# Performance work log

Measured on AMD Instinct MI355X. Metric: run time of the kernel, lower is better.

Reference implementation:

```python
import jax, jax.numpy as jnp
import numpy as np

EPS = 1e-5
B, C_IN, T_IN = 512, 12, 5000
NF, HID, LAT = 32, 64, 32


def setup_inputs() -> dict:
    key = jax.random.key(0)
    ks = jax.random.split(key, 12)
    inp = {
        "x": jax.random.normal(ks[0], (B, C_IN, T_IN), dtype=jnp.float32),
        # conv stack
        "conv1_w": jax.random.normal(ks[1], (32, C_IN, 50), dtype=jnp.float32) * 0.05,
        "conv1_b": jnp.zeros((32,), dtype=jnp.float32),
        "bn1_g": jnp.ones((32,), dtype=jnp.float32),
        "bn1_b": jnp.zeros((32,), dtype=jnp.float32),
        "conv2_w": jax.random.normal(ks[2], (NF, 32, 25), dtype=jnp.float32) * 0.05,
        "conv2_b": jnp.zeros((NF,), dtype=jnp.float32),
        "bn2_g": jnp.ones((NF,), dtype=jnp.float32),
        "bn2_b": jnp.zeros((NF,), dtype=jnp.float32),
        # input projection + layernorm
        "proj_w": jax.random.normal(ks[3], (LAT, NF), dtype=jnp.float32) * 0.1,
        "proj_b": jnp.zeros((LAT,), dtype=jnp.float32),
        "ln_g": jnp.ones((LAT,), dtype=jnp.float32),
        "ln_b": jnp.zeros((LAT,), dtype=jnp.float32),
        # PLRNN recurrence params
        "A": jnp.eye(LAT, dtype=jnp.float32) * 0.9,
        "W": jax.random.normal(ks[4], (LAT, HID), dtype=jnp.float32) * 0.1,
        "h_bias": jnp.zeros((HID,), dtype=jnp.float32),
        # output projection
        "out_w": jax.random.normal(ks[5], (LAT, LAT), dtype=jnp.float32) * 0.1,
        "out_b": jnp.zeros((LAT,), dtype=jnp.float32),
    }
    return inp


def _conv1d(x, w, b, stride):
    # x: [B, C, T], w: [O, I, K]
    y = jax.lax.conv_general_dilated(
        x, w, window_strides=(stride,), padding="VALID",
        dimension_numbers=("NCH", "OIH", "NCH"))
    return y + b[None, :, None]


def _batchnorm_train(x, g, b):
    # training-mode BN over (batch, time) per channel; x: [B, C, T]
    mean = jnp.mean(x, axis=(0, 2), keepdims=True)
    var = jnp.mean((x - mean) ** 2, axis=(0, 2), keepdims=True)
    return (x - mean) * jax.lax.rsqrt(var + EPS) * g[None, :, None] + b[None, :, None]


def _layernorm(x, g, b):
    mean = jnp.mean(x, axis=-1, keepdims=True)
    var = jnp.mean((x - mean) ** 2, axis=-1, keepdims=True)
    return (x - mean) * jax.lax.rsqrt(var + EPS) * g + b


def reference(x, conv1_w, conv1_b, bn1_g, bn1_b, conv2_w, conv2_b, bn2_g, bn2_b,
              proj_w, proj_b, ln_g, ln_b, A, W, h_bias, out_w, out_b):
    # conv front-end
    y = jax.nn.relu(_batchnorm_train(_conv1d(x, conv1_w, conv1_b, 10), bn1_g, bn1_b))
    y = jax.nn.relu(_batchnorm_train(_conv1d(y, conv2_w, conv2_b, 5), bn2_g, bn2_b))
    y = jnp.transpose(y, (0, 2, 1))  # [B, T, NF], T = 95

    # input projection + LN, vectorized over all timesteps
    xt = _layernorm(jnp.einsum("btf,lf->btl", y, proj_w) + proj_b, ln_g, ln_b)  # [B, T, L]
    xs = jnp.transpose(xt, (1, 0, 2))  # [T, B, L] for scan

    def step(h, x_t):
        # h: [B, L]
        linear = h @ A.T
        nonlinear = jax.nn.relu(h @ W + h_bias) @ W.T
        h_new = linear + nonlinear + x_t
        return h_new, h_new

    h0 = jnp.zeros((x.shape[0], A.shape[0]), dtype=x.dtype)
    _, outputs = jax.lax.scan(step, h0, xs)  # [T, B, L]

    pooled = jnp.mean(outputs, axis=0)  # [B, L]
    return pooled @ out_w.T + out_b
```

## Files before the change

### kernel.cpp

```cpp
#include <hip/hip_runtime.h>

#define NB    512
#define CIN   12
#define TIN   5000
#define C1    32
#define T1    496
#define T2    95
#define LATD  32
#define HIDD  64

#define OFS_STATS 0
#define OFS_W1P   256
#define OFS_W2P   19456
#define OFS_Y1    45056
#define OFS_Y2    8171520
#define OFS_XS    OFS_Y1

__global__ void prep_kernel(const float* __restrict__ w1, const float* __restrict__ w2,
                            float* __restrict__ ws) {
    int idx = blockIdx.x * 256 + threadIdx.x;
    if (idx < 256) ws[idx] = 0.f;
    int j = idx - 256;
    if (j >= 0 && j < 19200) {
        int ic = j / 1600, r = j % 1600, k = r / 32, oc = r % 32;
        ws[OFS_W1P + j] = w1[oc * 600 + ic * 50 + k];
    }
    int j2 = idx - 19456;
    if (j2 >= 0 && j2 < 25600) {
        int ic = j2 / 800, r = j2 % 800, k = r / 32, oc = r % 32;
        ws[OFS_W2P + j2] = w2[oc * 800 + ic * 25 + k];
    }
}

__global__ __launch_bounds__(128, 2) void conv1_kernel(const float* __restrict__ x,
                                                       const float* __restrict__ b1,
                                                       float* __restrict__ ws) {
    const float* w1p = ws + OFS_W1P;
    float* y1 = ws + OFS_Y1;
    float* stats = ws + OFS_STATS;
    int b  = blockIdx.x >> 1;
    int t0 = (blockIdx.x & 1) * 256;
    int tid = threadIdx.x;
    int ocg = tid & 3, tg = tid >> 2;
    int oc0 = ocg * 8, lt0 = tg * 8;
    int xbase = 82 * tg;

    __shared__ __align__(16) float xs_s[2][2664];
    __shared__ __align__(16) float ws_s[2][1600];
    __shared__ float sred[128];

    float acc[8][8];
#pragma unroll
    for (int a = 0; a < 8; ++a)
#pragma unroll
        for (int c = 0; c < 8; ++c) acc[a][c] = 0.f;

    const float* xb = x + (size_t)b * (CIN * TIN) + t0 * 10;
    int nvalid = TIN - t0 * 10;

    float4 px[6];
    float4 pw[4];

    auto fetch = [&](int ic) {
#pragma unroll
        for (int j = 0; j < 6; ++j) {
            int i = tid + j * 128;
            if (i < 650) {
                int src = 4 * i;
                const float* gp = xb + ic * TIN + src;
                float4 v;
                if (src + 4 <= nvalid) {
                    v = *(const float4*)gp;
                } else {
                    v.x = (src + 0 < nvalid) ? gp[0] : 0.f;
                    v.y = (src + 1 < nvalid) ? gp[1] : 0.f;
                    v.z = (src + 2 < nvalid) ? gp[2] : 0.f;
                    v.w = (src + 3 < nvalid) ? gp[3] : 0.f;
                }
                px[j] = v;
            }
        }
#pragma unroll
        for (int j = 0; j < 4; ++j) {
            int i = tid + j * 128;
            if (i < 400) pw[j] = *(const float4*)(w1p + ic * 1600 + 4 * i);
        }
    };

    fetch(0);
    for (int ic = 0; ic < CIN; ++ic) {
        int cur = ic & 1;
        __syncthreads();
#pragma unroll
        for (int j = 0; j < 6; ++j) {
            int i = tid + j * 128;
            if (i < 650) {
                int src = 4 * i;
                int dst = src + (i / 20) * 2;
                float2 lo; lo.x = px[j].x; lo.y = px[j].y;
                float2 hi; hi.x = px[j].z; hi.y = px[j].w;
                *(float2*)&xs_s[cur][dst]     = lo;
                *(float2*)&xs_s[cur][dst + 2] = hi;
            }
        }
#pragma unroll
        for (int j = 0; j < 4; ++j) {
            int i = tid + j * 128;
            if (i < 400) *(float4*)&ws_s[cur][4 * i] = pw[j];
        }
        if (ic + 1 < CIN) fetch(ic + 1);
        __syncthreads();

#pragma unroll 1
        for (int kp = 0; kp < 25; ++kp) {
            const int k = kp * 2;
            const float* wr = &ws_s[cur][k * 32 + oc0];
            float4 w00 = *(const float4*)wr;
            float4 w01 = *(const float4*)(wr + 4);
            float4 w10 = *(const float4*)(wr + 32);
            float4 w11 = *(const float4*)(wr + 36);
            float2 xv[8];
#pragma unroll
            for (int jt = 0; jt < 8; ++jt) {
                int r = jt * 10 + k;
                int ad = xbase + r + ((r >= 80) ? 2 : 0);
                xv[jt] = *(const float2*)&xs_s[cur][ad];
            }
            float wk[8]  = {w00.x, w00.y, w00.z, w00.w, w01.x, w01.y, w01.z, w01.w};
            float wk1[8] = {w10.x, w10.y, w10.z, w10.w, w11.x, w11.y, w11.z, w11.w};
#pragma unroll
            for (int jo = 0; jo < 8; ++jo)
#pragma unroll
                for (int jt = 0; jt < 8; ++jt)
                    acc[jo][jt] = fmaf(wk1[jo], xv[jt].y, fmaf(wk[jo], xv[jt].x, acc[jo][jt]));
        }
    }

    float bias[8];
#pragma unroll
    for (int jo = 0; jo < 8; ++jo) bias[jo] = b1[oc0 + jo];

    bool tvalid = (t0 + lt0) <= (T1 - 8);
    float psum[8], psq[8];
#pragma unroll
    for (int jo = 0; jo < 8; ++jo) {
        float s = 0.f, q = 0.f;
        if (tvalid) {
            float tmp[8];
#pragma unroll
            for (int jt = 0; jt < 8; ++jt) {
                float v = acc[jo][jt] + bias[jo];
                tmp[jt] = v; s += v; q = fmaf(v, v, q);
            }
            float* yrow = y1 + (size_t)(b * 32 + oc0 + jo) * T1 + t0 + lt0;
            float4 o0; o0.x = tmp[0]; o0.y = tmp[1]; o0.z = tmp[2]; o0.w = tmp[3];
            float4 o1; o1.x = tmp[4]; o1.y = tmp[5]; o1.z = tmp[6]; o1.w = tmp[7];
            *(float4*)yrow       = o0;
            *(float4*)(yrow + 4) = o1;
        }
        psum[jo] = s; psq[jo] = q;
    }
#pragma unroll
    for (int off = 32; off >= 4; off >>= 1) {
#pragma unroll
        for (int jo = 0; jo < 8; ++jo) {
            psum[jo] += __shfl_down(psum[jo], off, 64);
            psq[jo]  += __shfl_down(psq[jo],  off, 64);
        }
    }
    int lane = tid & 63, wvi = tid >> 6;
    if (lane < 4) {
#pragma unroll
        for (int jo = 0; jo < 8; ++jo) {
            sred[((wvi * 4 + lane) * 8 + jo) * 2 + 0] = psum[jo];
            sred[((wvi * 4 + lane) * 8 + jo) * 2 + 1] = psq[jo];
        }
    }
    __syncthreads();
    if (tid < 64) {
        int oc = tid >> 1, which = tid & 1;
        int og = oc >> 3, jo = oc & 7;
        float v = sred[((0 * 4 + og) * 8 + jo) * 2 + which] +
                  sred[((1 * 4 + og) * 8 + jo) * 2 + which];
        atomicAdd(&stats[which * 32 + oc], v);
    }
}

__global__ void bnstats_kernel(const float* __restrict__ g, const float* __restrict__ bparm,
                               float* __restrict__ ws, int base_in, int base_out, float invN) {
    int oc = threadIdx.x;
    if (oc < 32) {
        float* stats = ws + OFS_STATS;
        float mean = stats[base_in + oc] * invN;
        float var  = stats[base_in + 32 + oc] * invN - mean * mean;
        float s = g[oc] * rsqrtf(var + 1e-5f);
        stats[base_out + oc]      = s;
        stats[base_out + 32 + oc] = bparm[oc] - mean * s;
    }
}

__global__ __launch_bounds__(192, 2) void conv2_kernel(const float* __restrict__ b2,
                                                       float* __restrict__ ws) {
    const float* w2p = ws + OFS_W2P;
    const float* y1 = ws + OFS_Y1;
    float* y2 = ws + OFS_Y2;
    float* stats = ws + OFS_STATS;
    int b = blockIdx.x;
    int tid = threadIdx.x;
    int ocg = tid & 7, tg = tid >> 3;
    int oc0 = ocg * 4, lt0 = tg * 4;

    __shared__ __align__(16) float a1s[500];
    __shared__ __align__(16) float w2s[800];
    __shared__ float sred[192];

    float acc[4][4];
#pragma unroll
    for (int a = 0; a < 4; ++a)
#pragma unroll
        for (int c = 0; c < 4; ++c) acc[a][c] = 0.f;

    for (int ic = 0; ic < 32; ++ic) {
        __syncthreads();
        float s1  = stats[128 + ic];
        float sh1 = stats[160 + ic];
        const float* yrow = y1 + (size_t)(b * 32 + ic) * T1;
        for (int i = tid; i < 124; i += 192) {
            float4 v = *(const float4*)(yrow + 4 * i);
            v.x = fmaxf(fmaf(v.x, s1, sh1), 0.f);
            v.y = fmaxf(fmaf(v.y, s1, sh1), 0.f);
            v.z = fmaxf(fmaf(v.z, s1, sh1), 0.f);
            v.w = fmaxf(fmaf(v.w, s1, sh1), 0.f);
            *(float4*)&a1s[4 * i] = v;
        }
        for (int i = tid; i < 200; i += 192)
            *(float4*)&w2s[4 * i] = *(const float4*)(w2p + ic * 800 + 4 * i);
        __syncthreads();

#pragma unroll 1
        for (int kp = 0; kp < 12; ++kp) {
            const int k = kp * 2;
            float4 wA = *(const float4*)&w2s[k * 32 + oc0];
            float4 wB = *(const float4*)&w2s[(k + 1) * 32 + oc0];
            float x0[4], x1[4];
#pragma unroll
            for (int jt = 0; jt < 4; ++jt) {
                int a = 20 * tg + 5 * jt + k;
                x0[jt] = a1s[a]; x1[jt] = a1s[a + 1];
            }
            float wk[4]  = {wA.x, wA.y, wA.z, wA.w};
            float wk1[4] = {wB.x, wB.y, wB.z, wB.w};
#pragma unroll
            for (int jo = 0; jo < 4; ++jo)
#pragma unroll
                for (int jt = 0; jt < 4; ++jt)
                    acc[jo][jt] = fmaf(wk1[jo], x1[jt], fmaf(wk[jo], x0[jt], acc[jo][jt]));
        }
        float4 wT = *(const float4*)&w2s[24 * 32 + oc0];
        float wt[4] = {wT.x, wT.y, wT.z, wT.w};
#pragma unroll
        for (int jt = 0; jt < 4; ++jt) {
            float xt_ = a1s[20 * tg + 5 * jt + 24];
#pragma unroll
            for (int jo = 0; jo < 4; ++jo) acc[jo][jt] = fmaf(wt[jo], xt_, acc[jo][jt]);
        }
    }

    float bias[4];
#pragma unroll
    for (int jo = 0; jo < 4; ++jo) bias[jo] = b2[oc0 + jo];

    float psum[4], psq[4];
#pragma unroll
    for (int jo = 0; jo < 4; ++jo) {
        float s = 0.f, q = 0.f;
#pragma unroll
        for (int jt = 0; jt < 4; ++jt) {
            int t2 = lt0 + jt;
            if (t2 < T2) {
                float v = acc[jo][jt] + bias[jo];
                y2[(size_t)(b * 32 + oc0 + jo) * T2 + t2] = v;
                s += v; q = fmaf(v, v, q);
            }
        }
        psum[jo] = s; psq[jo] = q;
    }
#pragma unroll
    for (int off = 32; off >= 8; off >>= 1) {
#pragma unroll
        for (int jo = 0; jo < 4; ++jo) {
            psum[jo] += __shfl_down(psum[jo], off, 64);
            psq[jo]  += __shfl_down(psq[jo],  off, 64);
        }
    }
    int lane = tid & 63, wvi = tid >> 6;
    if (lane < 8) {
#pragma unroll
        for (int jo = 0; jo < 4; ++jo) {
            sred[((wvi * 8 + lane) * 4 + jo) * 2 + 0] = psum[jo];
            sred[((wvi * 8 + lane) * 4 + jo) * 2 + 1] = psq[jo];
        }
    }
    __syncthreads();
    if (tid < 64) {
        int oc = tid >> 1, which = tid & 1;
        int og = oc >> 2, jo = oc & 3;
        float v = 0.f;
#pragma unroll
        for (int w = 0; w < 3; ++w)
            v += sred[((w * 8 + og) * 4 + jo) * 2 + which];
        atomicAdd(&stats[64 + which * 32 + oc], v);
    }
}

__global__ __launch_bounds__(256, 2) void proj_kernel(const float* __restrict__ pw,
                                                      const float* __restrict__ pb,
                                                      const float* __restrict__ lng,
                                                      const float* __restrict__ lnb,
                                                      float* __restrict__ ws) {
    int b = blockIdx.x;
    int tid = threadIdx.x;
    __shared__ float a2s[3040];
    __shared__ float pws[1056];
    const float* stats = ws + OFS_STATS;
    const float* y2 = ws + OFS_Y2 + (size_t)b * (32 * T2);
    float* xsg = ws + OFS_XS;

    for (int f = 0; f < 32; ++f) {
        float s2  = stats[192 + f];
        float sh2 = stats[224 + f];
        if (tid < T2)
            a2s[f * T2 + tid] = fmaxf(fmaf(y2[f * T2 + tid], s2, sh2), 0.f);
    }
    for (int i = tid; i < 1024; i += 256)
        pws[(i >> 5) * 33 + (i & 31)] = pw[i];

    int l = tid & 31, ts = tid >> 5;
    float pbv = pb[l], lg = lng[l], lb = lnb[l];
    __syncthreads();

    for (int it = 0; it < 12; ++it) {
        int t = ts + 8 * it;
        if (t < T2) {
            float v = pbv;
#pragma unroll
            for (int f = 0; f < 32; ++f)
                v = fmaf(a2s[f * T2 + t], pws[l * 33 + f], v);
            float sum = v;
#pragma unroll
            for (int off = 16; off >= 1; off >>= 1) sum += __shfl_xor(sum, off, 64);
            float mean = sum * (1.f / 32.f);
            float d = v - mean;
            float q = d * d;
#pragma unroll
            for (int off = 16; off >= 1; off >>= 1) q += __shfl_xor(q, off, 64);
            float o = d * rsqrtf(q * (1.f / 32.f) + 1e-5f) * lg + lb;
            xsg[(size_t)t * (NB * 32) + b * 32 + l] = o;
        }
    }
}

__global__ __launch_bounds__(64)
__attribute__((amdgpu_waves_per_eu(1, 1)))
void scan_kernel(const float* __restrict__ Am,
                 const float* __restrict__ Wm,
                 const float* __restrict__ hbp,
                 const float* __restrict__ ow,
                 const float* __restrict__ ob,
                 const float* __restrict__ ws,
                 float* __restrict__ out) {
    int b = blockIdx.x;
    int lane = threadIdx.x;
    int l = lane & 31, half = lane >> 5;
    __shared__ __align__(16) float hs[32];
    __shared__ __align__(16) float hds[64];
    __shared__ float ows[1056];

    float Wc[32], WT[32], Ah[16];
#pragma unroll
    for (int j = 0; j < 32; ++j) Wc[j] = Wm[j * HIDD + lane];
#pragma unroll
    for (int m = 0; m < 32; ++m) WT[m] = Wm[l * HIDD + half * 32 + m];
#pragma unroll
    for (int j = 0; j < 16; ++j) Ah[j] = Am[l * 32 + half * 16 + j];
    float hbv = hbp[lane];
    for (int i = lane; i < 1024; i += 64)
        ows[(i >> 5) * 33 + (i & 31)] = ow[i];

    const float* xsg = ws + OFS_XS + b * 32;
    if (lane < 32) hs[l] = 0.f;
    float xv = xsg[l];
    float pool = 0.f;
    __syncthreads();

    for (int t = 0; t < T2; ++t) {
        __syncthreads();
        float4 hv[8];
#pragma unroll
        for (int q = 0; q < 8; ++q) hv[q] = *(const float4*)&hs[4 * q];
        float a0 = hbv, a1 = 0.f, a2 = 0.f, a3 = 0.f;
#pragma unroll
        for (int q = 0; q < 8; ++q) {
            a0 = fmaf(Wc[4 * q + 0], hv[q].x, a0);
            a1 = fmaf(Wc[4 * q + 1], hv[q].y, a1);
            a2 = fmaf(Wc[4 * q + 2], hv[q].z, a2);
            a3 = fmaf(Wc[4 * q + 3], hv[q].w, a3);
        }
        float hid = fmaxf((a0 + a1) + (a2 + a3), 0.f);
        float4 hl[4];
#pragma unroll
        for (int q = 0; q < 4; ++q) hl[q] = *(const float4*)&hs[half * 16 + 4 * q];
        float l0 = 0.f, l1 = 0.f;
#pragma unroll
        for (int q = 0; q < 4; ++q) {
            l0 = fmaf(Ah[4 * q + 0], hl[q].x, l0);
            l1 = fmaf(Ah[4 * q + 1], hl[q].y, l1);
            l0 = fmaf(Ah[4 * q + 2], hl[q].z, l0);
            l1 = fmaf(Ah[4 * q + 3], hl[q].w, l1);
        }
        float lin = l0 + l1;
        hds[lane] = hid;
        __syncthreads();
        float n0 = 0.f, n1 = 0.f, n2 = 0.f, n3 = 0.f;
#pragma unroll
        for (int q = 0; q < 8; ++q) {
            float4 d4 = *(const float4*)&hds[half * 32 + 4 * q];
            n0 = fmaf(WT[4 * q + 0], d4.x, n0);
            n1 = fmaf(WT[4 * q + 1], d4.y, n1);
            n2 = fmaf(WT[4 * q + 2], d4.z, n2);
            n3 = fmaf(WT[4 * q + 3], d4.w, n3);
        }
        float part = (n0 + n1) + (n2 + n3) + lin;
        part += __shfl_xor(part, 32, 64);
        float hnew = part + xv;
        pool += hnew;
        if (t + 1 < T2) xv = xsg[(size_t)(t + 1) * (NB * 32) + l];
        if (lane < 32) hs[l] = hnew;
    }

    __syncthreads();
    if (lane < 32) hs[l] = pool * (1.f / 95.f);
    __syncthreads();
    if (lane < 32) {
        float4 p0 = *(const float4*)&hs[0];
        float4 p1 = *(const float4*)&hs[4];
        float4 p2 = *(const float4*)&hs[8];
        float4 p3 = *(const float4*)&hs[12];
        float4 p4 = *(const float4*)&hs[16];
        float4 p5 = *(const float4*)&hs[20];
        float4 p6 = *(const float4*)&hs[24];
        float4 p7 = *(const float4*)&hs[28];
        float o = ob[l];
        const float* owr = &ows[l * 33];
        o = fmaf(owr[0],  p0.x, o); o = fmaf(owr[1],  p0.y, o);
        o = fmaf(owr[2],  p0.z, o); o = fmaf(owr[3],  p0.w, o);
        o = fmaf(owr[4],  p1.x, o); o = fmaf(owr[5],  p1.y, o);
        o = fmaf(owr[6],  p1.z, o); o = fmaf(owr[7],  p1.w, o);
        o = fmaf(owr[8],  p2.x, o); o = fmaf(owr[9],  p2.y, o);
        o = fmaf(owr[10], p2.z, o); o = fmaf(owr[11], p2.w, o);
        o = fmaf(owr[12], p3.x, o); o = fmaf(owr[13], p3.y, o);
        o = fmaf(owr[14], p3.z, o); o = fmaf(owr[15], p3.w, o);
        o = fmaf(owr[16], p4.x, o); o = fmaf(owr[17], p4.y, o);
        o = fmaf(owr[18], p4.z, o); o = fmaf(owr[19], p4.w, o);
        o = fmaf(owr[20], p5.x, o); o = fmaf(owr[21], p5.y, o);
        o = fmaf(owr[22], p5.z, o); o = fmaf(owr[23], p5.w, o);
        o = fmaf(owr[24], p6.x, o); o = fmaf(owr[25], p6.y, o);
        o = fmaf(owr[26], p6.z, o); o = fmaf(owr[27], p6.w, o);
        o = fmaf(owr[28], p7.x, o); o = fmaf(owr[29], p7.y, o);
        o = fmaf(owr[30], p7.z, o); o = fmaf(owr[31], p7.w, o);
        out[b * 32 + l] = o;
    }
}

extern "C" void kernel_launch(void* const* d_in, const int* in_sizes, int n_in,
                              void* d_out, int out_size, void* d_ws, size_t ws_size,
                              hipStream_t stream) {
    (void)in_sizes; (void)n_in; (void)out_size; (void)ws_size;
    const float* x   = (const float*)d_in[0];
    const float* w1  = (const float*)d_in[1];
    const float* b1  = (const float*)d_in[2];
    const float* g1  = (const float*)d_in[3];
    const float* be1 = (const float*)d_in[4];
    const float* w2  = (const float*)d_in[5];
    const float* b2  = (const float*)d_in[6];
    const float* g2  = (const float*)d_in[7];
    const float* be2 = (const float*)d_in[8];
    const float* pw  = (const float*)d_in[9];
    const float* pb  = (const float*)d_in[10];
    const float* lng = (const float*)d_in[11];
    const float* lnb = (const float*)d_in[12];
    const float* Am  = (const float*)d_in[13];
    const float* Wm  = (const float*)d_in[14];
    const float* hb  = (const float*)d_in[15];
    const float* ow  = (const float*)d_in[16];
    const float* ob  = (const float*)d_in[17];
    float* ws  = (float*)d_ws;
    float* out = (float*)d_out;

    prep_kernel<<<176, 256, 0, stream>>>(w1, w2, ws);
    conv1_kernel<<<1024, 128, 0, stream>>>(x, b1, ws);
    bnstats_kernel<<<1, 64, 0, stream>>>(g1, be1, ws, 0, 128, 1.f / 253952.f);
    conv2_kernel<<<512, 192, 0, stream>>>(b2, ws);
    bnstats_kernel<<<1, 64, 0, stream>>>(g2, be2, ws, 64, 192, 1.f / 48640.f);
    proj_kernel<<<512, 256, 0, stream>>>(pw, pb, lng, lnb, ws);
    scan_kernel<<<512, 64, 0, stream>>>(Am, Wm, hb, ow, ob, ws, out);
}
```

Baseline: 468.1 us.

## Widen conv1 blocks, double-buffer conv2 loads, fold BN stats into consumers

conv1 now runs 256 threads per block, each computing 4 timesteps instead of 8. This halves the per-thread accumulator count and doubles the number of waves available to hide latency. conv2 prefetches the next input channel's activations and weights into registers and double-buffers them in shared memory, which removes one dependency wait per channel. The two single-block bnstats kernels are removed and their scale/shift computation is folded into conv2 and proj, saving two launches at the cost of every block redundantly recomputing 32 values.

```diff
diff --git a/kernel.cpp b/kernel.cpp
--- a/kernel.cpp
+++ b/kernel.cpp
@@ -32,7 +32,7 @@
     }
 }
 
-__global__ __launch_bounds__(128, 2) void conv1_kernel(const float* __restrict__ x,
+__global__ __launch_bounds__(256, 2) void conv1_kernel(const float* __restrict__ x,
                                                        const float* __restrict__ b1,
                                                        float* __restrict__ ws) {
     const float* w1p = ws + OFS_W1P;
@@ -42,29 +42,30 @@
     int t0 = (blockIdx.x & 1) * 256;
     int tid = threadIdx.x;
     int ocg = tid & 3, tg = tid >> 2;
-    int oc0 = ocg * 8, lt0 = tg * 8;
-    int xbase = 82 * tg;
+    int oc0 = ocg * 8, lt0 = tg * 4;
+    int xbase  = 41 * tg - (tg & 1);
+    int thresh = (tg & 1) ? 40 : 127;
 
     __shared__ __align__(16) float xs_s[2][2664];
     __shared__ __align__(16) float ws_s[2][1600];
-    __shared__ float sred[128];
-
-    float acc[8][8];
+    __shared__ float sred[256];
+
+    float acc[8][4];
 #pragma unroll
     for (int a = 0; a < 8; ++a)
 #pragma unroll
-        for (int c = 0; c < 8; ++c) acc[a][c] = 0.f;
+        for (int c = 0; c < 4; ++c) acc[a][c] = 0.f;
 
     const float* xb = x + (size_t)b * (CIN * TIN) + t0 * 10;
     int nvalid = TIN - t0 * 10;
 
-    float4 px[6];
-    float4 pw[4];
+    float4 px[3];
+    float4 pw[2];
 
     auto fetch = [&](int ic) {
 #pragma unroll
-        for (int j = 0; j < 6; ++j) {
-            int i = tid + j * 128;
+        for (int j = 0; j < 3; ++j) {
+            int i = tid + j * 256;
             if (i < 650) {
                 int src = 4 * i;
                 const float* gp = xb + ic * TIN + src;
@@ -81,8 +82,8 @@
             }
         }
 #pragma unroll
-        for (int j = 0; j < 4; ++j) {
-            int i = tid + j * 128;
+        for (int j = 0; j < 2; ++j) {
+            int i = tid + j * 256;
             if (i < 400) pw[j] = *(const float4*)(w1p + ic * 1600 + 4 * i);
         }
     };
@@ -92,8 +93,8 @@
         int cur = ic & 1;
         __syncthreads();
 #pragma unroll
-        for (int j = 0; j < 6; ++j) {
-            int i = tid + j * 128;
+        for (int j = 0; j < 3; ++j) {
+            int i = tid + j * 256;
             if (i < 650) {
                 int src = 4 * i;
                 int dst = src + (i / 20) * 2;
@@ -104,8 +105,8 @@
             }
         }
 #pragma unroll
-        for (int j = 0; j < 4; ++j) {
-            int i = tid + j * 128;
+        for (int j = 0; j < 2; ++j) {
+            int i = tid + j * 256;
             if (i < 400) *(float4*)&ws_s[cur][4 * i] = pw[j];
         }
         if (ic + 1 < CIN) fetch(ic + 1);
@@ -119,11 +120,11 @@
             float4 w01 = *(const float4*)(wr + 4);
             float4 w10 = *(const float4*)(wr + 32);
             float4 w11 = *(const float4*)(wr + 36);
-            float2 xv[8];
-#pragma unroll
-            for (int jt = 0; jt < 8; ++jt) {
+            float2 xv[4];
+#pragma unroll
+            for (int jt = 0; jt < 4; ++jt) {
                 int r = jt * 10 + k;
-                int ad = xbase + r + ((r >= 80) ? 2 : 0);
+                int ad = xbase + r + ((r >= thresh) ? 2 : 0);
                 xv[jt] = *(const float2*)&xs_s[cur][ad];
             }
             float wk[8]  = {w00.x, w00.y, w00.z, w00.w, w01.x, w01.y, w01.z, w01.w};
@@ -131,7 +132,7 @@
 #pragma unroll
             for (int jo = 0; jo < 8; ++jo)
 #pragma unroll
-                for (int jt = 0; jt < 8; ++jt)
+                for (int jt = 0; jt < 4; ++jt)
                     acc[jo][jt] = fmaf(wk1[jo], xv[jt].y, fmaf(wk[jo], xv[jt].x, acc[jo][jt]));
         }
     }
@@ -140,23 +141,21 @@
 #pragma unroll
     for (int jo = 0; jo < 8; ++jo) bias[jo] = b1[oc0 + jo];
 
-    bool tvalid = (t0 + lt0) <= (T1 - 8);
+    bool tvalid = (t0 + lt0) <= (T1 - 4);
     float psum[8], psq[8];
 #pragma unroll
     for (int jo = 0; jo < 8; ++jo) {
         float s = 0.f, q = 0.f;
         if (tvalid) {
-            float tmp[8];
-#pragma unroll
-            for (int jt = 0; jt < 8; ++jt) {
+            float tmp[4];
+#pragma unroll
+            for (int jt = 0; jt < 4; ++jt) {
                 float v = acc[jo][jt] + bias[jo];
                 tmp[jt] = v; s += v; q = fmaf(v, v, q);
             }
             float* yrow = y1 + (size_t)(b * 32 + oc0 + jo) * T1 + t0 + lt0;
             float4 o0; o0.x = tmp[0]; o0.y = tmp[1]; o0.z = tmp[2]; o0.w = tmp[3];
-            float4 o1; o1.x = tmp[4]; o1.y = tmp[5]; o1.z = tmp[6]; o1.w = tmp[7];
-            *(float4*)yrow       = o0;
-            *(float4*)(yrow + 4) = o1;
+            *(float4*)yrow = o0;
         }
         psum[jo] = s; psq[jo] = q;
     }
@@ -180,26 +179,17 @@
     if (tid < 64) {
         int oc = tid >> 1, which = tid & 1;
         int og = oc >> 3, jo = oc & 7;
-        float v = sred[((0 * 4 + og) * 8 + jo) * 2 + which] +
-                  sred[((1 * 4 + og) * 8 + jo) * 2 + which];
+        float v = 0.f;
+#pragma unroll
+        for (int w = 0; w < 4; ++w)
+            v += sred[((w * 4 + og) * 8 + jo) * 2 + which];
         atomicAdd(&stats[which * 32 + oc], v);
     }
 }
 
-__global__ void bnstats_kernel(const float* __restrict__ g, const float* __restrict__ bparm,
-                               float* __restrict__ ws, int base_in, int base_out, float invN) {
-    int oc = threadIdx.x;
-    if (oc < 32) {
-        float* stats = ws + OFS_STATS;
-        float mean = stats[base_in + oc] * invN;
-        float var  = stats[base_in + 32 + oc] * invN - mean * mean;
-        float s = g[oc] * rsqrtf(var + 1e-5f);
-        stats[base_out + oc]      = s;
-        stats[base_out + 32 + oc] = bparm[oc] - mean * s;
-    }
-}
-
 __global__ __launch_bounds__(192, 2) void conv2_kernel(const float* __restrict__ b2,
+                                                       const float* __restrict__ g1,
+                                                       const float* __restrict__ be1,
                                                        float* __restrict__ ws) {
     const float* w2p = ws + OFS_W2P;
     const float* y1 = ws + OFS_Y1;
@@ -210,9 +200,18 @@
     int ocg = tid & 7, tg = tid >> 3;
     int oc0 = ocg * 4, lt0 = tg * 4;
 
-    __shared__ __align__(16) float a1s[500];
-    __shared__ __align__(16) float w2s[800];
+    __shared__ __align__(16) float a1s[2][500];
+    __shared__ __align__(16) float w2s[2][800];
     __shared__ float sred[192];
+    __shared__ float bns[64];
+
+    if (tid < 32) {
+        float mean = stats[tid] * (1.f / 253952.f);
+        float var  = stats[32 + tid] * (1.f / 253952.f) - mean * mean;
+        float s = g1[tid] * rsqrtf(var + 1e-5f);
+        bns[tid]      = s;
+        bns[32 + tid] = be1[tid] - mean * s;
+    }
 
     float acc[4][4];
 #pragma unroll
@@ -220,33 +219,42 @@
 #pragma unroll
         for (int c = 0; c < 4; ++c) acc[a][c] = 0.f;
 
+    float4 py, pw0, pw1;
+    auto fetch = [&](int ic) {
+        const float* yrow = y1 + (size_t)(b * 32 + ic) * T1;
+        if (tid < 124) py = *(const float4*)(yrow + 4 * tid);
+        pw0 = *(const float4*)(w2p + ic * 800 + 4 * tid);
+        if (tid < 8) pw1 = *(const float4*)(w2p + ic * 800 + 4 * (tid + 192));
+    };
+
+    fetch(0);
     for (int ic = 0; ic < 32; ++ic) {
+        int cur = ic & 1;
         __syncthreads();
-        float s1  = stats[128 + ic];
-        float sh1 = stats[160 + ic];
-        const float* yrow = y1 + (size_t)(b * 32 + ic) * T1;
-        for (int i = tid; i < 124; i += 192) {
-            float4 v = *(const float4*)(yrow + 4 * i);
+        if (tid < 124) {
+            float s1 = bns[ic], sh1 = bns[32 + ic];
+            float4 v = py;
             v.x = fmaxf(fmaf(v.x, s1, sh1), 0.f);
             v.y = fmaxf(fmaf(v.y, s1, sh1), 0.f);
             v.z = fmaxf(fmaf(v.z, s1, sh1), 0.f);
             v.w = fmaxf(fmaf(v.w, s1, sh1), 0.f);
-            *(float4*)&a1s[4 * i] = v;
-        }
-        for (int i = tid; i < 200; i += 192)
-            *(float4*)&w2s[4 * i] = *(const float4*)(w2p + ic * 800 + 4 * i);
+            *(float4*)&a1s[cur][4 * tid] = v;
+        }
+        *(float4*)&w2s[cur][4 * tid] = pw0;
+        if (tid < 8) *(float4*)&w2s[cur][4 * (tid + 192)] = pw1;
+        if (ic + 1 < 32) fetch(ic + 1);
         __syncthreads();
 
 #pragma unroll 1
         for (int kp = 0; kp < 12; ++kp) {
             const int k = kp * 2;
-            float4 wA = *(const float4*)&w2s[k * 32 + oc0];
-            float4 wB = *(const float4*)&w2s[(k + 1) * 32 + oc0];
+            float4 wA = *(const float4*)&w2s[cur][k * 32 + oc0];
+            float4 wB = *(const float4*)&w2s[cur][(k + 1) * 32 + oc0];
             float x0[4], x1[4];
 #pragma unroll
             for (int jt = 0; jt < 4; ++jt) {
                 int a = 20 * tg + 5 * jt + k;
-                x0[jt] = a1s[a]; x1[jt] = a1s[a + 1];
+                x0[jt] = a1s[cur][a]; x1[jt] = a1s[cur][a + 1];
             }
             float wk[4]  = {wA.x, wA.y, wA.z, wA.w};
             float wk1[4] = {wB.x, wB.y, wB.z, wB.w};
@@ -256,11 +264,11 @@
                 for (int jt = 0; jt < 4; ++jt)
                     acc[jo][jt] = fmaf(wk1[jo], x1[jt], fmaf(wk[jo], x0[jt], acc[jo][jt]));
         }
-        float4 wT = *(const float4*)&w2s[24 * 32 + oc0];
+        float4 wT = *(const float4*)&w2s[cur][24 * 32 + oc0];
         float wt[4] = {wT.x, wT.y, wT.z, wT.w};
 #pragma unroll
         for (int jt = 0; jt < 4; ++jt) {
-            float xt_ = a1s[20 * tg + 5 * jt + 24];
+            float xt_ = a1s[cur][20 * tg + 5 * jt + 24];
 #pragma unroll
             for (int jo = 0; jo < 4; ++jo) acc[jo][jt] = fmaf(wt[jo], xt_, acc[jo][jt]);
         }
@@ -313,7 +321,9 @@
     }
 }
 
-__global__ __launch_bounds__(256, 2) void proj_kernel(const float* __restrict__ pw,
+__global__ __launch_bounds__(256, 2) void proj_kernel(const float* __restrict__ g2,
+                                                      const float* __restrict__ be2,
+                                                      const float* __restrict__ pw,
                                                       const float* __restrict__ pb,
                                                       const float* __restrict__ lng,
                                                       const float* __restrict__ lnb,
@@ -322,13 +332,23 @@
     int tid = threadIdx.x;
     __shared__ float a2s[3040];
     __shared__ float pws[1056];
+    __shared__ float bns2[64];
     const float* stats = ws + OFS_STATS;
     const float* y2 = ws + OFS_Y2 + (size_t)b * (32 * T2);
     float* xsg = ws + OFS_XS;
 
+    if (tid < 32) {
+        float mean = stats[64 + tid] * (1.f / 48640.f);
+        float var  = stats[96 + tid] * (1.f / 48640.f) - mean * mean;
+        float s = g2[tid] * rsqrtf(var + 1e-5f);
+        bns2[tid]      = s;
+        bns2[32 + tid] = be2[tid] - mean * s;
+    }
+    __syncthreads();
+
     for (int f = 0; f < 32; ++f) {
-        float s2  = stats[192 + f];
-        float sh2 = stats[224 + f];
+        float s2  = bns2[f];
+        float sh2 = bns2[32 + f];
         if (tid < T2)
             a2s[f * T2 + tid] = fmaxf(fmaf(y2[f * T2 + tid], s2, sh2), 0.f);
     }
@@ -498,10 +518,8 @@
     float* out = (float*)d_out;
 
     prep_kernel<<<176, 256, 0, stream>>>(w1, w2, ws);
-    conv1_kernel<<<1024, 128, 0, stream>>>(x, b1, ws);
-    bnstats_kernel<<<1, 64, 0, stream>>>(g1, be1, ws, 0, 128, 1.f / 253952.f);
-    conv2_kernel<<<512, 192, 0, stream>>>(b2, ws);
-    bnstats_kernel<<<1, 64, 0, stream>>>(g2, be2, ws, 64, 192, 1.f / 48640.f);
-    proj_kernel<<<512, 256, 0, stream>>>(pw, pb, lng, lnb, ws);
+    conv1_kernel<<<1024, 256, 0, stream>>>(x, b1, ws);
+    conv2_kernel<<<512, 192, 0, stream>>>(b2, g1, be1, ws);
+    proj_kernel<<<512, 256, 0, stream>>>(g2, be2, pw, pb, lng, lnb, ws);
     scan_kernel<<<512, 64, 0, stream>>>(Am, Wm, hb, ow, ob, ws, out);
 }
```

Measured after the change: 458.3 us. 2.1% less time.
